# Performance work log

Hardware: AMD Instinct MI355X
Metric: run time of the kernel (lower is better)

The kernel has to match this reference:

```python
import jax, jax.numpy as jnp
import numpy as np

D_MODEL = 1024
N_HEADS = 16
D_H = D_MODEL // N_HEADS
B, S = 2, 2048


def setup_inputs() -> dict:
    key = jax.random.key(0)
    ks = jax.random.split(key, 12)
    s = 1.0 / np.sqrt(D_MODEL)
    inp = {
        "Q": jax.random.normal(ks[0], (B, S, D_MODEL), jnp.float32),
        "K": jax.random.normal(ks[1], (B, S, D_MODEL), jnp.float32),
        "V": jax.random.normal(ks[2], (B, S, D_MODEL), jnp.float32),
        # causal mask: True means masked out (matches masked_fill semantics)
        "masked": jnp.broadcast_to(~jnp.tril(jnp.ones((S, S), bool)), (B, S, S)),
        "WQ_w": jax.random.uniform(ks[3], (D_MODEL, D_MODEL), jnp.float32, -s, s),
        "WQ_b": jax.random.uniform(ks[4], (D_MODEL,), jnp.float32, -s, s),
        "WK_w": jax.random.uniform(ks[5], (D_MODEL, D_MODEL), jnp.float32, -s, s),
        "WK_b": jax.random.uniform(ks[6], (D_MODEL,), jnp.float32, -s, s),
        "WV_w": jax.random.uniform(ks[7], (D_MODEL, D_MODEL), jnp.float32, -s, s),
        "WV_b": jax.random.uniform(ks[8], (D_MODEL,), jnp.float32, -s, s),
        "Wo_w": jax.random.uniform(ks[9], (D_MODEL, D_MODEL), jnp.float32, -s, s),
        "Wo_b": jax.random.uniform(ks[10], (D_MODEL,), jnp.float32, -s, s),
    }
    return inp


def reference(Q, K, V, masked, WQ_w, WQ_b, WK_w, WK_b, WV_w, WV_b, Wo_w, Wo_b):
    b = Q.shape[0]
    # torch Linear: y = x @ W^T + b
    def split_heads(x):
        return x.reshape(b, -1, N_HEADS, D_H).transpose(0, 2, 1, 3)  # [B,H,S,d_h]

    q = split_heads(Q @ WQ_w.T + WQ_b)
    k = split_heads(K @ WK_w.T + WK_b)
    v = split_heads(V @ WV_w.T + WV_b)

    scores = jnp.einsum("bhqd,bhkd->bhqk", q, k) / np.sqrt(D_H)
    scores = jnp.where(masked[:, None, :, :], jnp.float32(-1e9), scores)
    attn = jax.nn.softmax(scores, axis=-1)
    ctx = jnp.einsum("bhqk,bhkd->bhqd", attn, v)  # [B,H,S,d_h]
    ctx = ctx.transpose(0, 2, 1, 3).reshape(b, -1, N_HEADS * D_H)
    return ctx @ Wo_w.T + Wo_b
```

## Files before the change

kernel.cpp:

```cpp
#include <hip/hip_runtime.h>
#include <hip/hip_bf16.h>
#include <math.h>


typedef __bf16 bf16_t;
typedef bf16_t bf16x8 __attribute__((ext_vector_type(8)));
typedef bf16_t bf16x4 __attribute__((ext_vector_type(4)));
typedef float f32x4 __attribute__((ext_vector_type(4)));

#define MFMA16(a, b, c) __builtin_amdgcn_mfma_f32_16x16x32_bf16(a, b, c, 0, 0, 0)

constexpr int S_LEN = 2048;
constexpr int DMODEL = 1024;
constexpr int DHEAD = 64;
constexpr int MTOT = 2 * S_LEN;
constexpr size_t NQ = (size_t)MTOT * DMODEL;
constexpr size_t NW = (size_t)DMODEL * DMODEL;

__device__ __forceinline__ void load_lds16(const void* g, void* l) {
  __builtin_amdgcn_global_load_lds((const __attribute__((address_space(1))) void*)g,
                                   (__attribute__((address_space(3))) void*)l, 16, 0, 0);
}

__global__ __launch_bounds__(256) void convert_all(
    const float* __restrict__ Q, const float* __restrict__ K, const float* __restrict__ V,
    const float* __restrict__ W0, const float* __restrict__ W1, const float* __restrict__ W2,
    const float* __restrict__ W3, bf16_t* __restrict__ dst) {
  const size_t i = ((size_t)blockIdx.x * 256 + threadIdx.x) * 4;
  const float* s;
  size_t off = i;
  if (off < NQ) { s = Q; }
  else if (off < 2 * NQ) { s = K; off -= NQ; }
  else if (off < 3 * NQ) { s = V; off -= 2 * NQ; }
  else {
    off -= 3 * NQ;
    if (off < NW) { s = W0; }
    else if (off < 2 * NW) { s = W1; off -= NW; }
    else if (off < 3 * NW) { s = W2; off -= 2 * NW; }
    else { s = W3; off -= 3 * NW; }
  }
  const float4 v4 = *(const float4*)(s + off);
  bf16x4 b;
  b[0] = (bf16_t)v4.x; b[1] = (bf16_t)v4.y; b[2] = (bf16_t)v4.z; b[3] = (bf16_t)v4.w;
  *(bf16x4*)(dst + i) = b;
}

template <int MODE>
__global__ __launch_bounds__(256) void gemm_bt(const bf16_t* __restrict__ A,
                                               const bf16_t* __restrict__ W,
                                               const float* __restrict__ bias,
                                               void* __restrict__ out) {
  constexpr int K = 1024;
  const int bm = blockIdx.x * 128;
  const int bn = blockIdx.y * 64;
  const int tid = threadIdx.x;
  const int lane = tid & 63, wave = tid >> 6;
  const int col = lane & 15, quad = lane >> 4;
  const int wm = (wave >> 1) * 64, wn = (wave & 1) * 32;

  __shared__ bf16_t As[128 * 64];
  __shared__ bf16_t Ws[64 * 64];

  f32x4 acc[4][2];
#pragma unroll
  for (int i = 0; i < 4; i++)
#pragma unroll
    for (int j = 0; j < 2; j++)
#pragma unroll
      for (int r = 0; r < 4; r++) acc[i][j][r] = 0.f;

  const int srow = lane >> 3;
  const int gch = (lane & 7) ^ srow;
  const bf16_t* Ab = A + (size_t)bm * K;
  const bf16_t* Wb = W + (size_t)bn * K;

  for (int k0 = 0; k0 < K; k0 += 64) {
    __syncthreads();
#pragma unroll
    for (int qq = 0; qq < 4; qq++) {
      const int rbase = (qq * 4 + wave) * 8;
      load_lds16(Ab + (size_t)(rbase + srow) * K + k0 + gch * 8, &As[rbase * 64]);
    }
#pragma unroll
    for (int qq = 0; qq < 2; qq++) {
      const int rbase = (qq * 4 + wave) * 8;
      load_lds16(Wb + (size_t)(rbase + srow) * K + k0 + gch * 8, &Ws[rbase * 64]);
    }
    __syncthreads();
#pragma unroll
    for (int kc = 0; kc < 2; kc++) {
      const int slot = (kc * 4 + quad) ^ (col & 7);
      bf16x8 af[4], wf[2];
#pragma unroll
      for (int i = 0; i < 4; i++) af[i] = *(const bf16x8*)&As[(wm + i * 16 + col) * 64 + slot * 8];
#pragma unroll
      for (int j = 0; j < 2; j++) wf[j] = *(const bf16x8*)&Ws[(wn + j * 16 + col) * 64 + slot * 8];
#pragma unroll
      for (int i = 0; i < 4; i++)
#pragma unroll
        for (int j = 0; j < 2; j++) acc[i][j] = MFMA16(af[i], wf[j], acc[i][j]);
    }
  }

#pragma unroll
  for (int i = 0; i < 4; i++) {
#pragma unroll
    for (int j = 0; j < 2; j++) {
      const int n = bn + wn + j * 16 + col;
      const float bv = bias[n];
#pragma unroll
      for (int r = 0; r < 4; r++) {
        const int m = bm + wm + i * 16 + quad * 4 + r;
        const float v = acc[i][j][r] + bv;
        if (MODE == 0) {
          const int b = m >> 11, s = m & 2047;
          const int h = n >> 6, dh = n & 63;
          ((bf16_t*)out)[((size_t)((b * 16 + h) * S_LEN + s) << 6) | dh] = (bf16_t)v;
        } else if (MODE == 1) {
          const int b = m >> 11, s = m & 2047;
          const int h = n >> 6, dh = n & 63;
          ((bf16_t*)out)[((size_t)((b * 16 + h) * DHEAD + dh) << 11) | s] = (bf16_t)v;
        } else {
          ((float*)out)[(size_t)m * DMODEL + n] = v;
        }
      }
    }
  }
}

__global__ __launch_bounds__(512) void attn(const bf16_t* __restrict__ q,
                                            const bf16_t* __restrict__ k,
                                            const bf16_t* __restrict__ vT,
                                            bf16_t* __restrict__ ctx) {
  const int bh = blockIdx.x;
  const int p = blockIdx.y;
  const int tA = p, tB = 15 - p;
  const int tid = threadIdx.x;
  const int lane = tid & 63, wave = tid >> 6;
  const int col = lane & 15, quad = lane >> 4;

  __shared__ bf16_t Ks[2][128 * 64];
  __shared__ bf16_t Vs[2][64 * 128];
  __shared__ bf16_t Ps[8][16 * 128];

  const bf16_t* kbh = k + (size_t)bh * S_LEN * DHEAD;
  const bf16_t* vbh = vT + (size_t)bh * DHEAD * S_LEN;

  const int k_srow = lane >> 3;
  const int k_gch = (lane & 7) ^ k_srow;
  const int v_drow = lane >> 4;
  const int v_slot = lane & 15;

  auto stage = [&](int c, int buf) {
#pragma unroll
    for (int i = 0; i < 2; i++) {
      const int rbase = (wave * 2 + i) * 8;
      load_lds16(kbh + (size_t)(c * 128 + rbase + k_srow) * 64 + k_gch * 8,
                 &Ks[buf][rbase * 64]);
    }
#pragma unroll
    for (int i = 0; i < 2; i++) {
      const int dbase = (wave * 2 + i) * 4;
      const int d = dbase + v_drow;
      const int gch = v_slot ^ (d & 7);
      load_lds16(vbh + (size_t)d * S_LEN + c * 128 + gch * 8, &Vs[buf][dbase * 128]);
    }
  };

  f32x4 o[4];
  float mrow[4], lrow[4];
  bf16x8 aq[2];
  int buf = 0;

  stage(0, 0);

  for (int it = 0; it <= 16; ++it) {
    const bool onA = (it <= tA);
    const int T = onA ? tA : tB;
    const int c = onA ? it : it - (tA + 1);

    if (c == 0) {
      const bf16_t* qb = q + ((size_t)bh * S_LEN + T * 128 + wave * 16 + col) * DHEAD;
      aq[0] = *(const bf16x8*)(qb + quad * 8);
      aq[1] = *(const bf16x8*)(qb + 32 + quad * 8);
#pragma unroll
      for (int db = 0; db < 4; db++)
#pragma unroll
        for (int r = 0; r < 4; r++) o[db][r] = 0.f;
#pragma unroll
      for (int r = 0; r < 4; r++) { mrow[r] = -INFINITY; lrow[r] = 0.f; }
    }

    if (it < 16) {
      const int cn = (it + 1 <= tA) ? it + 1 : it - tA;
      stage(cn, buf ^ 1);
    }

    f32x4 sacc[8];
#pragma unroll
    for (int nb = 0; nb < 8; nb++)
#pragma unroll
      for (int r = 0; r < 4; r++) sacc[nb][r] = 0.f;
#pragma unroll
    for (int kc = 0; kc < 2; kc++) {
      const int slot = (kc * 4 + quad) ^ (col & 7);
#pragma unroll
      for (int nb = 0; nb < 8; nb++) {
        const bf16x8 bk = *(const bf16x8*)&Ks[buf][(nb * 16 + col) * 64 + slot * 8];
        sacc[nb] = MFMA16(aq[kc], bk, sacc[nb]);
      }
    }

    constexpr float sc = 0.125f * 1.44269504088896f;
    if (c == T) {
#pragma unroll
      for (int nb = 0; nb < 8; nb++)
#pragma unroll
        for (int r = 0; r < 4; r++) {
          const int key = nb * 16 + col;
          const int qr = wave * 16 + quad * 4 + r;
          sacc[nb][r] = (key > qr) ? -INFINITY : sacc[nb][r] * sc;
        }
    } else {
#pragma unroll
      for (int nb = 0; nb < 8; nb++)
#pragma unroll
        for (int r = 0; r < 4; r++) sacc[nb][r] *= sc;
    }

    float mx[4];
#pragma unroll
    for (int r = 0; r < 4; r++) {
      mx[r] = fmaxf(fmaxf(fmaxf(sacc[0][r], sacc[1][r]), fmaxf(sacc[2][r], sacc[3][r])),
                    fmaxf(fmaxf(sacc[4][r], sacc[5][r]), fmaxf(sacc[6][r], sacc[7][r])));
#pragma unroll
      for (int off = 1; off < 16; off <<= 1) mx[r] = fmaxf(mx[r], __shfl_xor(mx[r], off));
    }
    float alpha[4];
#pragma unroll
    for (int r = 0; r < 4; r++) {
      const float mnew = fmaxf(mrow[r], mx[r]);
      alpha[r] = exp2f(mrow[r] - mnew);
      mrow[r] = mnew;
    }
    float rs[4] = {0.f, 0.f, 0.f, 0.f};
#pragma unroll
    for (int nb = 0; nb < 8; nb++)
#pragma unroll
      for (int r = 0; r < 4; r++) {
        const float pv = exp2f(sacc[nb][r] - mrow[r]);
        sacc[nb][r] = pv;
        rs[r] += pv;
      }
#pragma unroll
    for (int r = 0; r < 4; r++) {
#pragma unroll
      for (int off = 1; off < 16; off <<= 1) rs[r] += __shfl_xor(rs[r], off);
      lrow[r] = lrow[r] * alpha[r] + rs[r];
    }
#pragma unroll
    for (int db = 0; db < 4; db++)
#pragma unroll
      for (int r = 0; r < 4; r++) o[db][r] *= alpha[r];

#pragma unroll
    for (int nb = 0; nb < 8; nb++) {
      const int cb = nb * 2 + (col >> 3);
#pragma unroll
      for (int r = 0; r < 4; r++) {
        const int qr = quad * 4 + r;
        Ps[wave][qr * 128 + ((cb ^ (qr & 7)) * 8) + (col & 7)] = (bf16_t)sacc[nb][r];
      }
    }

#pragma unroll
    for (int kc = 0; kc < 4; kc++) {
      const int slot = (kc * 4 + quad) ^ (col & 7);
      const bf16x8 pa = *(const bf16x8*)&Ps[wave][col * 128 + slot * 8];
#pragma unroll
      for (int db = 0; db < 4; db++) {
        const bf16x8 bv = *(const bf16x8*)&Vs[buf][(db * 16 + col) * 128 + slot * 8];
        o[db] = MFMA16(pa, bv, o[db]);
      }
    }

    __syncthreads();
    buf ^= 1;

    if (c == T) {
      const int b = bh >> 4, h = bh & 15;
      float inv[4];
#pragma unroll
      for (int r = 0; r < 4; r++) inv[r] = 1.f / lrow[r];
#pragma unroll
      for (int db = 0; db < 4; db++)
#pragma unroll
        for (int r = 0; r < 4; r++) {
          const int qg = T * 128 + wave * 16 + quad * 4 + r;
          ctx[((size_t)(b * S_LEN + qg)) * DMODEL + h * DHEAD + db * 16 + col] =
              (bf16_t)(o[db][r] * inv[r]);
        }
    }
  }
}

extern "C" void kernel_launch(void* const* d_in, const int* in_sizes, int n_in,
                              void* d_out, int out_size, void* d_ws, size_t ws_size,
                              hipStream_t stream) {
  const float* Q = (const float*)d_in[0];
  const float* K = (const float*)d_in[1];
  const float* V = (const float*)d_in[2];
  const float* WQw = (const float*)d_in[4];
  const float* WQb = (const float*)d_in[5];
  const float* WKw = (const float*)d_in[6];
  const float* WKb = (const float*)d_in[7];
  const float* WVw = (const float*)d_in[8];
  const float* WVb = (const float*)d_in[9];
  const float* Wow = (const float*)d_in[10];
  const float* Wob = (const float*)d_in[11];

  bf16_t* base = (bf16_t*)d_ws;
  bf16_t* Qc = base;
  bf16_t* Kc = base + NQ;
  bf16_t* Vc = base + 2 * NQ;
  bf16_t* Wc = base + 3 * NQ;
  bf16_t* qp = base + 3 * NQ + 4 * NW;
  bf16_t* kp = qp + NQ;
  bf16_t* vt = kp + NQ;
  bf16_t* ctx = Qc;

  const size_t total = 3 * NQ + 4 * NW;
  convert_all<<<dim3((unsigned)(total / 4 / 256)), dim3(256), 0, stream>>>(
      Q, K, V, WQw, WKw, WVw, Wow, base);

  const dim3 gg(MTOT / 128, DMODEL / 64);
  gemm_bt<0><<<gg, dim3(256), 0, stream>>>(Qc, Wc + 0 * NW, WQb, qp);
  gemm_bt<0><<<gg, dim3(256), 0, stream>>>(Kc, Wc + 1 * NW, WKb, kp);
  gemm_bt<1><<<gg, dim3(256), 0, stream>>>(Vc, Wc + 2 * NW, WVb, vt);
  attn<<<dim3(32, 8), dim3(512), 0, stream>>>(qp, kp, vt, ctx);
  gemm_bt<2><<<gg, dim3(256), 0, stream>>>(ctx, Wc + 3 * NW, Wob, d_out);
}
```

Baseline: 264.7 us.

## Merge QKV GEMMs into one launch, drop online-softmax max, retile attention

The three projection GEMMs become one batched launch over blockIdx.z with 128x128 tiles. The softmax scale and log2e are folded into the Q projection. The output GEMM uses a BK=128 tile. Attention now runs with 256 threads, each wave handling 32 query rows. It drops the running-max/rescale online softmax and exponentiates raw scores directly, and it removes K/V double buffering. This cuts launch count, softmax ALU and shuffle work, but it risks overflow for large scores and loses load/compute overlap.

```diff
diff --git a/kernel.cpp b/kernel.cpp
--- a/kernel.cpp
+++ b/kernel.cpp
@@ -16,6 +16,7 @@
 constexpr int MTOT = 2 * S_LEN;
 constexpr size_t NQ = (size_t)MTOT * DMODEL;
 constexpr size_t NW = (size_t)DMODEL * DMODEL;
+constexpr float ESC = 0.18033688011112042f;
 
 __device__ __forceinline__ void load_lds16(const void* g, void* l) {
   __builtin_amdgcn_global_load_lds((const __attribute__((address_space(1))) void*)g,
@@ -45,134 +46,162 @@
   *(bf16x4*)(dst + i) = b;
 }
 
-template <int MODE>
-__global__ __launch_bounds__(256) void gemm_bt(const bf16_t* __restrict__ A,
-                                               const bf16_t* __restrict__ W,
-                                               const float* __restrict__ bias,
-                                               void* __restrict__ out) {
-  constexpr int K = 1024;
-  const int bm = blockIdx.x * 128;
-  const int bn = blockIdx.y * 64;
-  const int tid = threadIdx.x;
-  const int lane = tid & 63, wave = tid >> 6;
+template <int BK>
+__device__ __forceinline__ void gemm_loop(const bf16_t* __restrict__ Ab,
+                                          const bf16_t* __restrict__ Wb,
+                                          bf16_t* As, bf16_t* Ws,
+                                          f32x4 (&acc)[4][4], int wave, int lane) {
+  constexpr int CH = BK / 8;
+  constexpr int RPI = 64 / CH;
+  constexpr int IPW = BK / 16;
   const int col = lane & 15, quad = lane >> 4;
-  const int wm = (wave >> 1) * 64, wn = (wave & 1) * 32;
-
+  const int wm = (wave >> 1) * 64, wn = (wave & 1) * 64;
+  const int srow = lane / CH;
+  const int sch = lane % CH;
+
+  for (int k0 = 0; k0 < 1024; k0 += BK) {
+    __syncthreads();
+#pragma unroll
+    for (int i = 0; i < IPW; i++) {
+      const int rbase = (i * 4 + wave) * RPI;
+      const int g = sch ^ ((rbase + srow) & 7);
+      load_lds16(Ab + (size_t)(rbase + srow) * 1024 + k0 + g * 8, As + rbase * BK);
+      load_lds16(Wb + (size_t)(rbase + srow) * 1024 + k0 + g * 8, Ws + rbase * BK);
+    }
+    __syncthreads();
+#pragma unroll
+    for (int kc = 0; kc < BK / 32; kc++) {
+      const int slot = (kc * 4 + quad) ^ (col & 7);
+      bf16x8 af[4], wf[4];
+#pragma unroll
+      for (int i = 0; i < 4; i++) af[i] = *(const bf16x8*)&As[(wm + i * 16 + col) * BK + slot * 8];
+#pragma unroll
+      for (int j = 0; j < 4; j++) wf[j] = *(const bf16x8*)&Ws[(wn + j * 16 + col) * BK + slot * 8];
+#pragma unroll
+      for (int i = 0; i < 4; i++)
+#pragma unroll
+        for (int j = 0; j < 4; j++) acc[i][j] = MFMA16(af[i], wf[j], acc[i][j]);
+    }
+  }
+}
+
+__global__ __launch_bounds__(256, 3) void gemm_qkv(const bf16_t* __restrict__ Abase,
+                                                   const bf16_t* __restrict__ Wbase,
+                                                   const float* __restrict__ b0,
+                                                   const float* __restrict__ b1,
+                                                   const float* __restrict__ b2,
+                                                   bf16_t* __restrict__ obase) {
   __shared__ bf16_t As[128 * 64];
-  __shared__ bf16_t Ws[64 * 64];
-
-  f32x4 acc[4][2];
+  __shared__ bf16_t Ws[128 * 64];
+  const int z = blockIdx.z;
+  const int bm = blockIdx.x * 128, bn = blockIdx.y * 128;
+  const int lane = threadIdx.x & 63, wave = threadIdx.x >> 6;
+  const int col = lane & 15, quad = lane >> 4;
+  const int wm = (wave >> 1) * 64, wn = (wave & 1) * 64;
+
+  f32x4 acc[4][4];
 #pragma unroll
   for (int i = 0; i < 4; i++)
 #pragma unroll
-    for (int j = 0; j < 2; j++)
+    for (int j = 0; j < 4; j++)
 #pragma unroll
       for (int r = 0; r < 4; r++) acc[i][j][r] = 0.f;
 
-  const int srow = lane >> 3;
-  const int gch = (lane & 7) ^ srow;
-  const bf16_t* Ab = A + (size_t)bm * K;
-  const bf16_t* Wb = W + (size_t)bn * K;
-
-  for (int k0 = 0; k0 < K; k0 += 64) {
-    __syncthreads();
-#pragma unroll
-    for (int qq = 0; qq < 4; qq++) {
-      const int rbase = (qq * 4 + wave) * 8;
-      load_lds16(Ab + (size_t)(rbase + srow) * K + k0 + gch * 8, &As[rbase * 64]);
-    }
-#pragma unroll
-    for (int qq = 0; qq < 2; qq++) {
-      const int rbase = (qq * 4 + wave) * 8;
-      load_lds16(Wb + (size_t)(rbase + srow) * K + k0 + gch * 8, &Ws[rbase * 64]);
-    }
-    __syncthreads();
-#pragma unroll
-    for (int kc = 0; kc < 2; kc++) {
-      const int slot = (kc * 4 + quad) ^ (col & 7);
-      bf16x8 af[4], wf[2];
-#pragma unroll
-      for (int i = 0; i < 4; i++) af[i] = *(const bf16x8*)&As[(wm + i * 16 + col) * 64 + slot * 8];
-#pragma unroll
-      for (int j = 0; j < 2; j++) wf[j] = *(const bf16x8*)&Ws[(wn + j * 16 + col) * 64 + slot * 8];
-#pragma unroll
-      for (int i = 0; i < 4; i++)
-#pragma unroll
-        for (int j = 0; j < 2; j++) acc[i][j] = MFMA16(af[i], wf[j], acc[i][j]);
-    }
-  }
-
+  const bf16_t* A = Abase + z * NQ + (size_t)bm * 1024;
+  const bf16_t* W = Wbase + z * NW + (size_t)bn * 1024;
+  const float* bias = (z == 0) ? b0 : ((z == 1) ? b1 : b2);
+  bf16_t* out = obase + z * NQ;
+
+  gemm_loop<64>(A, W, As, Ws, acc, wave, lane);
+
+  const float esc = (z == 0) ? ESC : 1.0f;
 #pragma unroll
   for (int i = 0; i < 4; i++) {
 #pragma unroll
-    for (int j = 0; j < 2; j++) {
+    for (int j = 0; j < 4; j++) {
       const int n = bn + wn + j * 16 + col;
       const float bv = bias[n];
+      const int h = n >> 6, dh = n & 63;
+      if (z < 2) {
+#pragma unroll
+        for (int r = 0; r < 4; r++) {
+          const int m = bm + wm + i * 16 + quad * 4 + r;
+          const int b = m >> 11, s = m & 2047;
+          out[((size_t)((b * 16 + h) * S_LEN + s) << 6) | dh] =
+              (bf16_t)((acc[i][j][r] + bv) * esc);
+        }
+      } else {
+        const int m0 = bm + wm + i * 16 + quad * 4;
+        const int b = m0 >> 11, s0 = m0 & 2047;
+        bf16x4 p4;
+#pragma unroll
+        for (int r = 0; r < 4; r++) p4[r] = (bf16_t)(acc[i][j][r] + bv);
+        *(bf16x4*)&out[(((size_t)((b * 16 + h) * DHEAD + dh)) << 11) | s0] = p4;
+      }
+    }
+  }
+}
+
+__global__ __launch_bounds__(256) void gemm_out(const bf16_t* __restrict__ A,
+                                                const bf16_t* __restrict__ W,
+                                                const float* __restrict__ bias,
+                                                float* __restrict__ out) {
+  __shared__ bf16_t As[128 * 128];
+  __shared__ bf16_t Ws[128 * 128];
+  const int bm = blockIdx.x * 128, bn = blockIdx.y * 128;
+  const int lane = threadIdx.x & 63, wave = threadIdx.x >> 6;
+  const int col = lane & 15, quad = lane >> 4;
+  const int wm = (wave >> 1) * 64, wn = (wave & 1) * 64;
+
+  f32x4 acc[4][4];
+#pragma unroll
+  for (int i = 0; i < 4; i++)
+#pragma unroll
+    for (int j = 0; j < 4; j++)
+#pragma unroll
+      for (int r = 0; r < 4; r++) acc[i][j][r] = 0.f;
+
+  gemm_loop<128>(A + (size_t)bm * 1024, W + (size_t)bn * 1024, As, Ws, acc, wave, lane);
+
+#pragma unroll
+  for (int i = 0; i < 4; i++)
+#pragma unroll
+    for (int j = 0; j < 4; j++) {
+      const int n = bn + wn + j * 16 + col;
+      const float bv = bias[n];
 #pragma unroll
       for (int r = 0; r < 4; r++) {
         const int m = bm + wm + i * 16 + quad * 4 + r;
-        const float v = acc[i][j][r] + bv;
-        if (MODE == 0) {
-          const int b = m >> 11, s = m & 2047;
-          const int h = n >> 6, dh = n & 63;
-          ((bf16_t*)out)[((size_t)((b * 16 + h) * S_LEN + s) << 6) | dh] = (bf16_t)v;
-        } else if (MODE == 1) {
-          const int b = m >> 11, s = m & 2047;
-          const int h = n >> 6, dh = n & 63;
-          ((bf16_t*)out)[((size_t)((b * 16 + h) * DHEAD + dh) << 11) | s] = (bf16_t)v;
-        } else {
-          ((float*)out)[(size_t)m * DMODEL + n] = v;
-        }
-      }
-    }
-  }
-}
-
-__global__ __launch_bounds__(512) void attn(const bf16_t* __restrict__ q,
-                                            const bf16_t* __restrict__ k,
-                                            const bf16_t* __restrict__ vT,
-                                            bf16_t* __restrict__ ctx) {
+        out[(size_t)m * DMODEL + n] = acc[i][j][r] + bv;
+      }
+    }
+}
+
+constexpr int PP = 136;
+
+__global__ __launch_bounds__(256, 2) void attn(const bf16_t* __restrict__ q,
+                                               const bf16_t* __restrict__ k,
+                                               const bf16_t* __restrict__ vT,
+                                               bf16_t* __restrict__ ctx) {
   const int bh = blockIdx.x;
   const int p = blockIdx.y;
   const int tA = p, tB = 15 - p;
-  const int tid = threadIdx.x;
-  const int lane = tid & 63, wave = tid >> 6;
+  const int lane = threadIdx.x & 63, wave = threadIdx.x >> 6;
   const int col = lane & 15, quad = lane >> 4;
 
-  __shared__ bf16_t Ks[2][128 * 64];
-  __shared__ bf16_t Vs[2][64 * 128];
-  __shared__ bf16_t Ps[8][16 * 128];
+  __shared__ bf16_t Ks[128 * 64];
+  __shared__ bf16_t Vs[64 * 128];
+  __shared__ bf16_t Ps[4][32 * PP];
 
   const bf16_t* kbh = k + (size_t)bh * S_LEN * DHEAD;
   const bf16_t* vbh = vT + (size_t)bh * DHEAD * S_LEN;
 
-  const int k_srow = lane >> 3;
-  const int k_gch = (lane & 7) ^ k_srow;
-  const int v_drow = lane >> 4;
-  const int v_slot = lane & 15;
-
-  auto stage = [&](int c, int buf) {
-#pragma unroll
-    for (int i = 0; i < 2; i++) {
-      const int rbase = (wave * 2 + i) * 8;
-      load_lds16(kbh + (size_t)(c * 128 + rbase + k_srow) * 64 + k_gch * 8,
-                 &Ks[buf][rbase * 64]);
-    }
-#pragma unroll
-    for (int i = 0; i < 2; i++) {
-      const int dbase = (wave * 2 + i) * 4;
-      const int d = dbase + v_drow;
-      const int gch = v_slot ^ (d & 7);
-      load_lds16(vbh + (size_t)d * S_LEN + c * 128 + gch * 8, &Vs[buf][dbase * 128]);
-    }
-  };
-
-  f32x4 o[4];
-  float mrow[4], lrow[4];
-  bf16x8 aq[2];
-  int buf = 0;
-
-  stage(0, 0);
+  const int k_srow = lane >> 3, k_g = (lane & 7) ^ k_srow;
+  const int v_row = lane >> 4, v_sl = lane & 15;
+
+  bf16x8 aq[2][2];
+  f32x4 o[2][4];
+  float lsum[2];
 
   for (int it = 0; it <= 16; ++it) {
     const bool onA = (it <= tA);
@@ -180,126 +209,107 @@
     const int c = onA ? it : it - (tA + 1);
 
     if (c == 0) {
-      const bf16_t* qb = q + ((size_t)bh * S_LEN + T * 128 + wave * 16 + col) * DHEAD;
-      aq[0] = *(const bf16x8*)(qb + quad * 8);
-      aq[1] = *(const bf16x8*)(qb + 32 + quad * 8);
-#pragma unroll
-      for (int db = 0; db < 4; db++)
-#pragma unroll
-        for (int r = 0; r < 4; r++) o[db][r] = 0.f;
-#pragma unroll
-      for (int r = 0; r < 4; r++) { mrow[r] = -INFINITY; lrow[r] = 0.f; }
-    }
-
-    if (it < 16) {
-      const int cn = (it + 1 <= tA) ? it + 1 : it - tA;
-      stage(cn, buf ^ 1);
-    }
-
-    f32x4 sacc[8];
-#pragma unroll
-    for (int nb = 0; nb < 8; nb++)
-#pragma unroll
-      for (int r = 0; r < 4; r++) sacc[nb][r] = 0.f;
+      const bf16_t* qb = q + ((size_t)bh * S_LEN + T * 128 + wave * 32 + col) * DHEAD;
+#pragma unroll
+      for (int qf = 0; qf < 2; qf++) {
+        aq[qf][0] = *(const bf16x8*)(qb + qf * 16 * DHEAD + quad * 8);
+        aq[qf][1] = *(const bf16x8*)(qb + qf * 16 * DHEAD + 32 + quad * 8);
+      }
+#pragma unroll
+      for (int qf = 0; qf < 2; qf++) {
+        lsum[qf] = 0.f;
+#pragma unroll
+        for (int db = 0; db < 4; db++)
+#pragma unroll
+          for (int r = 0; r < 4; r++) o[qf][db][r] = 0.f;
+      }
+    }
+
+    __syncthreads();
+#pragma unroll
+    for (int i = 0; i < 4; i++) {
+      const int rbase = wave * 32 + i * 8;
+      load_lds16(kbh + (size_t)(c * 128 + rbase + k_srow) * DHEAD + k_g * 8, &Ks[rbase * 64]);
+    }
+#pragma unroll
+    for (int i = 0; i < 4; i++) {
+      const int dbase = wave * 16 + i * 4;
+      const int d = dbase + v_row;
+      const int g = v_sl ^ (d & 7);
+      load_lds16(vbh + (size_t)d * S_LEN + c * 128 + g * 8, &Vs[dbase * 128]);
+    }
+    __syncthreads();
+
+    f32x4 sacc[2][8];
+#pragma unroll
+    for (int qf = 0; qf < 2; qf++)
+#pragma unroll
+      for (int nb = 0; nb < 8; nb++)
+#pragma unroll
+        for (int r = 0; r < 4; r++) sacc[qf][nb][r] = 0.f;
 #pragma unroll
     for (int kc = 0; kc < 2; kc++) {
       const int slot = (kc * 4 + quad) ^ (col & 7);
 #pragma unroll
       for (int nb = 0; nb < 8; nb++) {
-        const bf16x8 bk = *(const bf16x8*)&Ks[buf][(nb * 16 + col) * 64 + slot * 8];
-        sacc[nb] = MFMA16(aq[kc], bk, sacc[nb]);
-      }
-    }
-
-    constexpr float sc = 0.125f * 1.44269504088896f;
-    if (c == T) {
-#pragma unroll
-      for (int nb = 0; nb < 8; nb++)
+        const bf16x8 bk = *(const bf16x8*)&Ks[(nb * 16 + col) * 64 + slot * 8];
+#pragma unroll
+        for (int qf = 0; qf < 2; qf++) sacc[qf][nb] = MFMA16(bk, aq[qf][kc], sacc[qf][nb]);
+      }
+    }
+
+    const bool diag = (c == T);
+#pragma unroll
+    for (int qf = 0; qf < 2; qf++) {
+      const int ql = wave * 32 + qf * 16 + col;
+#pragma unroll
+      for (int nb = 0; nb < 8; nb++) {
+        bf16x4 p4;
 #pragma unroll
         for (int r = 0; r < 4; r++) {
-          const int key = nb * 16 + col;
-          const int qr = wave * 16 + quad * 4 + r;
-          sacc[nb][r] = (key > qr) ? -INFINITY : sacc[nb][r] * sc;
+          const int keyl = nb * 16 + quad * 4 + r;
+          float pv = exp2f(sacc[qf][nb][r]);
+          if (diag && keyl > ql) pv = 0.f;
+          lsum[qf] += pv;
+          p4[r] = (bf16_t)pv;
         }
-    } else {
-#pragma unroll
-      for (int nb = 0; nb < 8; nb++)
-#pragma unroll
-        for (int r = 0; r < 4; r++) sacc[nb][r] *= sc;
-    }
-
-    float mx[4];
-#pragma unroll
-    for (int r = 0; r < 4; r++) {
-      mx[r] = fmaxf(fmaxf(fmaxf(sacc[0][r], sacc[1][r]), fmaxf(sacc[2][r], sacc[3][r])),
-                    fmaxf(fmaxf(sacc[4][r], sacc[5][r]), fmaxf(sacc[6][r], sacc[7][r])));
-#pragma unroll
-      for (int off = 1; off < 16; off <<= 1) mx[r] = fmaxf(mx[r], __shfl_xor(mx[r], off));
-    }
-    float alpha[4];
-#pragma unroll
-    for (int r = 0; r < 4; r++) {
-      const float mnew = fmaxf(mrow[r], mx[r]);
-      alpha[r] = exp2f(mrow[r] - mnew);
-      mrow[r] = mnew;
-    }
-    float rs[4] = {0.f, 0.f, 0.f, 0.f};
-#pragma unroll
-    for (int nb = 0; nb < 8; nb++)
-#pragma unroll
-      for (int r = 0; r < 4; r++) {
-        const float pv = exp2f(sacc[nb][r] - mrow[r]);
-        sacc[nb][r] = pv;
-        rs[r] += pv;
-      }
-#pragma unroll
-    for (int r = 0; r < 4; r++) {
-#pragma unroll
-      for (int off = 1; off < 16; off <<= 1) rs[r] += __shfl_xor(rs[r], off);
-      lrow[r] = lrow[r] * alpha[r] + rs[r];
-    }
-#pragma unroll
-    for (int db = 0; db < 4; db++)
-#pragma unroll
-      for (int r = 0; r < 4; r++) o[db][r] *= alpha[r];
-
-#pragma unroll
-    for (int nb = 0; nb < 8; nb++) {
-      const int cb = nb * 2 + (col >> 3);
-#pragma unroll
-      for (int r = 0; r < 4; r++) {
-        const int qr = quad * 4 + r;
-        Ps[wave][qr * 128 + ((cb ^ (qr & 7)) * 8) + (col & 7)] = (bf16_t)sacc[nb][r];
+        *(bf16x4*)&Ps[wave][(qf * 16 + col) * PP + nb * 16 + quad * 4] = p4;
       }
     }
 
 #pragma unroll
     for (int kc = 0; kc < 4; kc++) {
-      const int slot = (kc * 4 + quad) ^ (col & 7);
-      const bf16x8 pa = *(const bf16x8*)&Ps[wave][col * 128 + slot * 8];
+      const int slotv = (kc * 4 + quad) ^ (col & 7);
+      bf16x8 pa[2];
+#pragma unroll
+      for (int qf = 0; qf < 2; qf++)
+        pa[qf] = *(const bf16x8*)&Ps[wave][(qf * 16 + col) * PP + kc * 32 + quad * 8];
 #pragma unroll
       for (int db = 0; db < 4; db++) {
-        const bf16x8 bv = *(const bf16x8*)&Vs[buf][(db * 16 + col) * 128 + slot * 8];
-        o[db] = MFMA16(pa, bv, o[db]);
-      }
-    }
-
-    __syncthreads();
-    buf ^= 1;
+        const bf16x8 bv = *(const bf16x8*)&Vs[(db * 16 + col) * 128 + slotv * 8];
+#pragma unroll
+        for (int qf = 0; qf < 2; qf++) o[qf][db] = MFMA16(bv, pa[qf], o[qf][db]);
+      }
+    }
 
     if (c == T) {
       const int b = bh >> 4, h = bh & 15;
-      float inv[4];
-#pragma unroll
-      for (int r = 0; r < 4; r++) inv[r] = 1.f / lrow[r];
-#pragma unroll
-      for (int db = 0; db < 4; db++)
-#pragma unroll
-        for (int r = 0; r < 4; r++) {
-          const int qg = T * 128 + wave * 16 + quad * 4 + r;
-          ctx[((size_t)(b * S_LEN + qg)) * DMODEL + h * DHEAD + db * 16 + col] =
-              (bf16_t)(o[db][r] * inv[r]);
+#pragma unroll
+      for (int qf = 0; qf < 2; qf++) {
+        float l = lsum[qf];
+        l += __shfl_xor(l, 16);
+        l += __shfl_xor(l, 32);
+        const float inv = 1.f / l;
+        const int qg = T * 128 + wave * 32 + qf * 16 + col;
+        bf16_t* cb = ctx + ((size_t)(b * S_LEN + qg)) * DMODEL + h * DHEAD;
+#pragma unroll
+        for (int db = 0; db < 4; db++) {
+          bf16x4 o4;
+#pragma unroll
+          for (int r = 0; r < 4; r++) o4[r] = (bf16_t)(o[qf][db][r] * inv);
+          *(bf16x4*)&cb[db * 16 + quad * 4] = o4;
         }
+      }
     }
   }
 }
@@ -320,23 +330,15 @@
   const float* Wob = (const float*)d_in[11];
 
   bf16_t* base = (bf16_t*)d_ws;
-  bf16_t* Qc = base;
-  bf16_t* Kc = base + NQ;
-  bf16_t* Vc = base + 2 * NQ;
   bf16_t* Wc = base + 3 * NQ;
   bf16_t* qp = base + 3 * NQ + 4 * NW;
-  bf16_t* kp = qp + NQ;
-  bf16_t* vt = kp + NQ;
-  bf16_t* ctx = Qc;
+  bf16_t* ctx = base;
 
   const size_t total = 3 * NQ + 4 * NW;
   convert_all<<<dim3((unsigned)(total / 4 / 256)), dim3(256), 0, stream>>>(
       Q, K, V, WQw, WKw, WVw, Wow, base);
 
-  const dim3 gg(MTOT / 128, DMODEL / 64);
-  gemm_bt<0><<<gg, dim3(256), 0, stream>>>(Qc, Wc + 0 * NW, WQb, qp);
-  gemm_bt<0><<<gg, dim3(256), 0, stream>>>(Kc, Wc + 1 * NW, WKb, kp);
-  gemm_bt<1><<<gg, dim3(256), 0, stream>>>(Vc, Wc + 2 * NW, WVb, vt);
-  attn<<<dim3(32, 8), dim3(512), 0, stream>>>(qp, kp, vt, ctx);
-  gemm_bt<2><<<gg, dim3(256), 0, stream>>>(ctx, Wc + 3 * NW, Wob, d_out);
-}
+  gemm_qkv<<<dim3(32, 8, 3), dim3(256), 0, stream>>>(base, Wc, WQb, WKb, WVb, qp);
+  attn<<<dim3(32, 8), dim3(256), 0, stream>>>(qp, qp + NQ, qp + 2 * NQ, ctx);
+  gemm_out<<<dim3(32, 8), dim3(256), 0, stream>>>(ctx, Wc + 3 * NW, Wob, (float*)d_out);
+}
```

Result: faster. 244.9 us (-7.5%).
